# Kernel optimization log

Hardware: AMD Instinct MI355X
Metric: run time of the kernel (lower is better)

The kernel has to match this reference:

```python
import jax, jax.numpy as jnp
import numpy as np

DIMS, HEAD = 1024, 16
HD = DIMS // HEAD  # 64
MAX_ITER = 3
B, T = 4, 2048


def _ln(x, w, eps=1e-5):
    # torch LayerNorm with bias=False
    m = jnp.mean(x, axis=-1, keepdims=True)
    v = jnp.var(x, axis=-1, keepdims=True)
    return (x - m) * jax.lax.rsqrt(v + eps) * w


def setup_inputs() -> dict:
    key = jax.random.key(0)
    ks = jax.random.split(key, 10)
    n = lambda k, s: jax.random.normal(k, s, jnp.float32) * 0.02
    z = lambda s: jnp.zeros(s, jnp.float32)
    o = lambda s: jnp.ones(s, jnp.float32)
    return {
        "x": jax.random.normal(ks[0], (B, T, DIMS), jnp.float32),
        "Wq": n(ks[1], (DIMS, DIMS)), "bq": z((DIMS,)),
        "Wk": n(ks[2], (DIMS, DIMS)),
        "Wv": n(ks[3], (DIMS, DIMS)), "bv": z((DIMS,)),
        "Wo": n(ks[4], (DIMS, DIMS)), "bo": z((DIMS,)),
        "lna_w": o((DIMS,)), "lnc_w": o((HD,)), "lnd_w": o((HD,)),
        "Wlq": n(ks[5], (HD, HD)), "blq": z((HD,)),
        "Wlk": n(ks[6], (HD, HD)), "blk": z((HD,)),
        "Wlv": n(ks[7], (HD, HD)), "blv": z((HD,)),
        "temp": jnp.float32(1.0),
        "threshold": jnp.float32(0.01),
        "factor": jnp.float32(0.1),
    }


def reference(x, Wq, bq, Wk, Wv, bv, Wo, bo, lna_w, lnc_w, lnd_w,
              Wlq, blq, Wlk, blk, Wlv, blv, temp, threshold, factor):
    Bn, Tn, D = x.shape
    H, hd = HEAD, HD
    # .item() in torch detaches these params
    temp0 = jax.lax.stop_gradient(temp)
    thr = jax.lax.stop_gradient(threshold)
    fac = jax.lax.stop_gradient(factor)

    scale = hd ** -0.25
    xn = _ln(x, lna_w)
    q = (xn @ Wq.T + bq) * scale
    k = (xn @ Wk.T) * scale  # no bias
    v = xn @ Wv.T + bv
    shp = lambda t: t.reshape(Bn, Tn, H, hd).transpose(0, 2, 1, 3)  # (B,H,T,hd)
    q, k, v = shp(q), shp(k), shp(v)

    # eff_span = min(qcur.shape[1], k.shape[1]) == head dim of (B,H,T,hd)
    E = H
    sm_scale = 1.0 / float(np.sqrt(hd))

    qcur, kcur, vcur = q, k, v
    prev = jnp.zeros_like(q)
    attn_out = jnp.zeros_like(q)
    done = jnp.asarray(False)
    for it in range(MAX_ITER):
        ql = qcur[:, :, :E] @ Wlq.T + blq  # (B,H,E,hd)
        kl = kcur[:, :, :E] @ Wlk.T + blk
        vl = vcur[:, :, :E] @ Wlv.T + blv
        t_it = temp0 + 0.005 * it
        tscale = jnp.where((t_it != 1.0) & (t_it > 0), jax.lax.rsqrt(t_it), 1.0)
        qs = _ln(ql, lnc_w) * tscale
        ks_ = _ln(kl, lnd_w)
        logits = jnp.einsum('bhqd,bhkd->bhqk', qs, ks_) * sm_scale
        ai = jnp.einsum('bhqk,bhkd->bhqd', jax.nn.softmax(logits, axis=-1), vl)
        iter_out = jnp.zeros_like(qcur).at[:, :, :E].set(ai)
        diff = jnp.mean(jnp.abs(iter_out - prev))
        attn_out = jnp.where(done, attn_out, iter_out)  # freeze after break
        done = done | ((diff < thr + fac * diff) & (it > 0))
        prev = iter_out
        qcur = qcur + iter_out
        kcur, vcur = kl, vl

    out = attn_out.transpose(0, 2, 1, 3).reshape(Bn, Tn, D)
    return out @ Wo.T + bo
```

## Files before the change

kernel.cpp:

```cpp
#include <hip/hip_runtime.h>
#include <math.h>

#define WS_XN    0
#define WS_QKVP  65536
#define WS_DIFF  1638400
#define WS_AI1   1638404
#define WS_AI2   1703940
#define WS_WOP   1769476
#define WS_WT    2293764

__device__ __forceinline__ float4 f4zero() { return make_float4(0.f, 0.f, 0.f, 0.f); }
__device__ __forceinline__ float4 f4add(float4 a, float4 b) {
    return make_float4(a.x + b.x, a.y + b.y, a.z + b.z, a.w + b.w);
}
__device__ __forceinline__ float4 f4fma(float s, float4 a, float4 c) {
    return make_float4(fmaf(s, a.x, c.x), fmaf(s, a.y, c.y),
                       fmaf(s, a.z, c.z), fmaf(s, a.w, c.w));
}
__device__ __forceinline__ float dot4acc(float4 a, float4 b, float acc) {
    acc = fmaf(a.x, b.x, acc); acc = fmaf(a.y, b.y, acc);
    acc = fmaf(a.z, b.z, acc); acc = fmaf(a.w, b.w, acc);
    return acc;
}

__device__ __forceinline__ void gemm_lds(const float* __restrict__ ldsA, int tq,
                                         const float* __restrict__ ldsW, int dq,
                                         float acc[4][4]) {
#pragma unroll 8
    for (int k = 0; k < 64; ++k) {
        float4 a4 = *(const float4*)&ldsA[k * 20 + 4 * tq];
        float4 b4 = *(const float4*)&ldsW[k * 64 + 4 * dq];
        float av[4] = { a4.x, a4.y, a4.z, a4.w };
#pragma unroll
        for (int i = 0; i < 4; i++) {
            acc[i][0] = fmaf(av[i], b4.x, acc[i][0]);
            acc[i][1] = fmaf(av[i], b4.y, acc[i][1]);
            acc[i][2] = fmaf(av[i], b4.z, acc[i][2]);
            acc[i][3] = fmaf(av[i], b4.w, acc[i][3]);
        }
    }
}

__global__ __launch_bounds__(256) void k_ln(const float* __restrict__ x,
                                            const float* __restrict__ lna,
                                            const float* __restrict__ Wlq,
                                            const float* __restrict__ Wlk,
                                            const float* __restrict__ Wlv,
                                            float* __restrict__ xn,
                                            float* __restrict__ wt,
                                            float* __restrict__ diffg) {
    if (blockIdx.x >= 64) {
        int m = blockIdx.x - 64;
        const float* W = (m == 0) ? Wlq : (m == 1) ? Wlk : Wlv;
        float* dst = wt + m * 4096;
        for (int i = threadIdx.x; i < 4096; i += 256) {
            int k = i >> 6, d = i & 63;
            dst[i] = W[d * 64 + k];
        }
        return;
    }
    int r = blockIdx.x;
    int b = r >> 4, t = r & 15;
    if (blockIdx.x == 0 && threadIdx.x == 0) diffg[0] = 0.f;
    const float* row = x + (size_t)(b * 2048 + t) * 1024;
    int tid = threadIdx.x;
    float4 xv = *(const float4*)&row[tid * 4];
    float s1 = xv.x + xv.y + xv.z + xv.w;
    float s2 = xv.x * xv.x + xv.y * xv.y + xv.z * xv.z + xv.w * xv.w;
    for (int off = 32; off; off >>= 1) {
        s1 += __shfl_xor(s1, off);
        s2 += __shfl_xor(s2, off);
    }
    __shared__ float ssum[4], ssq[4];
    int wv = tid >> 6, lane = tid & 63;
    if (lane == 0) { ssum[wv] = s1; ssq[wv] = s2; }
    __syncthreads();
    float tot = ssum[0] + ssum[1] + ssum[2] + ssum[3];
    float tq  = ssq[0] + ssq[1] + ssq[2] + ssq[3];
    float m   = tot * (1.0f / 1024.0f);
    float var = tq * (1.0f / 1024.0f) - m * m;
    float rs  = rsqrtf(var + 1e-5f);
    float4 w4 = *(const float4*)&lna[tid * 4];
    float4 o  = make_float4((xv.x - m) * rs * w4.x, (xv.y - m) * rs * w4.y,
                            (xv.z - m) * rs * w4.z, (xv.w - m) * rs * w4.w);
    *(float4*)&xn[r * 1024 + tid * 4] = o;
}

__global__ __launch_bounds__(256) void k_qkv(const float* __restrict__ xn,
                                             const float* __restrict__ Wq,
                                             const float* __restrict__ Wk,
                                             const float* __restrict__ Wv,
                                             float* __restrict__ qkvp) {
    int ct  = blockIdx.x;
    int ksl = blockIdx.y;
    int m   = ct >> 5;
    const float* W = (m == 0) ? Wq : (m == 1) ? Wk : Wv;
    int j0 = (ct & 31) * 32;
    int k0 = ksl * 128;
    __shared__ float At[64][132];
    __shared__ float Bt[32][132];
    int tid = threadIdx.x;
    for (int i = tid; i < 2048; i += 256) {
        int r = i >> 5, kk = (i & 31) << 2;
        *(float4*)&At[r][kk] = *(const float4*)&xn[r * 1024 + k0 + kk];
    }
    for (int i = tid; i < 1024; i += 256) {
        int r = i >> 5, kk = (i & 31) << 2;
        *(float4*)&Bt[r][kk] = *(const float4*)&W[(size_t)(j0 + r) * 1024 + k0 + kk];
    }
    __syncthreads();
    int rg = tid >> 4, cg = tid & 15;
    float acc[4][2];
#pragma unroll
    for (int i = 0; i < 4; i++) { acc[i][0] = 0.f; acc[i][1] = 0.f; }
    for (int k = 0; k < 128; k += 4) {
        float4 b0 = *(float4*)&Bt[cg * 2 + 0][k];
        float4 b1 = *(float4*)&Bt[cg * 2 + 1][k];
#pragma unroll
        for (int i = 0; i < 4; i++) {
            float4 a = *(float4*)&At[rg * 4 + i][k];
            acc[i][0] = dot4acc(a, b0, acc[i][0]);
            acc[i][1] = dot4acc(a, b1, acc[i][1]);
        }
    }
    float* dst = qkvp + (size_t)ksl * 196608;
    int colg = ct * 32 + cg * 2;
#pragma unroll
    for (int i = 0; i < 4; i++) {
        *(float2*)&dst[(rg * 4 + i) * 3072 + colg] = make_float2(acc[i][0], acc[i][1]);
    }
}

__global__ __launch_bounds__(256, 1) void k_iter(
        const float* __restrict__ qkvp, const float* __restrict__ wt,
        const float* __restrict__ bq,  const float* __restrict__ bv,
        const float* __restrict__ lnc, const float* __restrict__ lnd,
        const float* __restrict__ blq, const float* __restrict__ blk_,
        const float* __restrict__ blv, const float* __restrict__ temp,
        float* __restrict__ ai1g, float* __restrict__ ai2g,
        float* __restrict__ diffg) {
    __shared__ __align__(16) float wS[12288];
    __shared__ __align__(16) float qcT[64 * 20];
    __shared__ __align__(16) float kcT[64 * 20];
    __shared__ __align__(16) float vcT[64 * 20];
    __shared__ __align__(16) float qsR[16 * 68];
    __shared__ __align__(16) float ksR[16 * 68];
    __shared__ __align__(16) float vlR[16 * 68];
    __shared__ float dred[4];

    int tid  = threadIdx.x;
    int b    = blockIdx.x >> 4, h = blockIdx.x & 15;
    int wv   = tid >> 6, lane = tid & 63;
    float tempv = temp[0];

    int tq = lane >> 4, dq = lane & 15;
    int t2 = tid >> 4,  u  = tid & 15;
    int rowi2 = b * 16 + t2, col2 = h * 64 + u * 4;

#pragma unroll
    for (int j = 0; j < 12; ++j) {
        int idx = (tid + j * 256) * 4;
        *(float4*)&wS[idx] = *(const float4*)&wt[idx];
    }

    {
        const float SCALE = 0.35355339059327378f;
        const float* P = qkvp + rowi2 * 3072 + col2;
        float4 q4 = f4zero(), k4 = f4zero(), v4 = f4zero();
#pragma unroll
        for (int sl = 0; sl < 8; sl++) {
            const float* Ps = P + (size_t)sl * 196608;
            q4 = f4add(q4, *(const float4*)&Ps[0]);
            k4 = f4add(k4, *(const float4*)&Ps[1024]);
            v4 = f4add(v4, *(const float4*)&Ps[2048]);
        }
        float4 bq4 = *(const float4*)&bq[col2];
        float4 bv4 = *(const float4*)&bv[col2];
        float qv[4] = { (q4.x + bq4.x) * SCALE, (q4.y + bq4.y) * SCALE,
                        (q4.z + bq4.z) * SCALE, (q4.w + bq4.w) * SCALE };
        float kv[4] = { k4.x * SCALE, k4.y * SCALE, k4.z * SCALE, k4.w * SCALE };
        float vv[4] = { v4.x + bv4.x, v4.y + bv4.y, v4.z + bv4.z, v4.w + bv4.w };
#pragma unroll
        for (int c = 0; c < 4; c++) {
            qcT[(u * 4 + c) * 20 + t2] = qv[c];
            kcT[(u * 4 + c) * 20 + t2] = kv[c];
            vcT[(u * 4 + c) * 20 + t2] = vv[c];
        }
    }
    __syncthreads();

    float4 ai0 = f4zero();
    float  dlocal = 0.f;

#pragma unroll 1
    for (int it = 0; it < 3; ++it) {
        float t_it = tempv + 0.005f * (float)it;
        float tsc  = (t_it != 1.0f && t_it > 0.0f) ? rsqrtf(t_it) : 1.0f;

        if (wv == 0) {
            float acc[4][4];
#pragma unroll
            for (int i = 0; i < 4; i++)
#pragma unroll
                for (int j = 0; j < 4; j++) acc[i][j] = 0.f;
            gemm_lds(qcT, tq, wS, dq, acc);
            float4 bb = *(const float4*)&blq[4 * dq];
            float4 lw = *(const float4*)&lnc[4 * dq];
#pragma unroll
            for (int i = 0; i < 4; i++) {
                acc[i][0] += bb.x; acc[i][1] += bb.y;
                acc[i][2] += bb.z; acc[i][3] += bb.w;
                float s1 = acc[i][0] + acc[i][1] + acc[i][2] + acc[i][3];
                float s2 = acc[i][0]*acc[i][0] + acc[i][1]*acc[i][1]
                         + acc[i][2]*acc[i][2] + acc[i][3]*acc[i][3];
                for (int off = 8; off; off >>= 1) {
                    s1 += __shfl_xor(s1, off); s2 += __shfl_xor(s2, off);
                }
                float m  = s1 * (1.0f / 64.0f);
                float vr = s2 * (1.0f / 64.0f) - m * m;
                float rs = rsqrtf(vr + 1e-5f) * tsc;
                float4 o = make_float4((acc[i][0] - m) * rs * lw.x,
                                       (acc[i][1] - m) * rs * lw.y,
                                       (acc[i][2] - m) * rs * lw.z,
                                       (acc[i][3] - m) * rs * lw.w);
                *(float4*)&qsR[(4 * tq + i) * 68 + 4 * dq] = o;
            }
        } else if (wv == 1) {
            float acc[4][4];
#pragma unroll
            for (int i = 0; i < 4; i++)
#pragma unroll
                for (int j = 0; j < 4; j++) acc[i][j] = 0.f;
            gemm_lds(kcT, tq, wS + 4096, dq, acc);
            float4 bb = *(const float4*)&blk_[4 * dq];
#pragma unroll
            for (int i = 0; i < 4; i++) {
                acc[i][0] += bb.x; acc[i][1] += bb.y;
                acc[i][2] += bb.z; acc[i][3] += bb.w;
            }
#pragma unroll
            for (int j = 0; j < 4; j++) {
                float4 cv = make_float4(acc[0][j], acc[1][j], acc[2][j], acc[3][j]);
                *(float4*)&kcT[(4 * dq + j) * 20 + 4 * tq] = cv;
            }
            float4 lw = *(const float4*)&lnd[4 * dq];
#pragma unroll
            for (int i = 0; i < 4; i++) {
                float s1 = acc[i][0] + acc[i][1] + acc[i][2] + acc[i][3];
                float s2 = acc[i][0]*acc[i][0] + acc[i][1]*acc[i][1]
                         + acc[i][2]*acc[i][2] + acc[i][3]*acc[i][3];
                for (int off = 8; off; off >>= 1) {
                    s1 += __shfl_xor(s1, off); s2 += __shfl_xor(s2, off);
                }
                float m  = s1 * (1.0f / 64.0f);
                float vr = s2 * (1.0f / 64.0f) - m * m;
                float rs = rsqrtf(vr + 1e-5f);
                float4 o = make_float4((acc[i][0] - m) * rs * lw.x,
                                       (acc[i][1] - m) * rs * lw.y,
                                       (acc[i][2] - m) * rs * lw.z,
                                       (acc[i][3] - m) * rs * lw.w);
                *(float4*)&ksR[(4 * tq + i) * 68 + 4 * dq] = o;
            }
        } else if (wv == 2) {
            float acc[4][4];
#pragma unroll
            for (int i = 0; i < 4; i++)
#pragma unroll
                for (int j = 0; j < 4; j++) acc[i][j] = 0.f;
            gemm_lds(vcT, tq, wS + 8192, dq, acc);
            float4 bb = *(const float4*)&blv[4 * dq];
#pragma unroll
            for (int i = 0; i < 4; i++) {
                acc[i][0] += bb.x; acc[i][1] += bb.y;
                acc[i][2] += bb.z; acc[i][3] += bb.w;
                *(float4*)&vlR[(4 * tq + i) * 68 + 4 * dq] =
                    make_float4(acc[i][0], acc[i][1], acc[i][2], acc[i][3]);
            }
#pragma unroll
            for (int j = 0; j < 4; j++) {
                float4 cv = make_float4(acc[0][j], acc[1][j], acc[2][j], acc[3][j]);
                *(float4*)&vcT[(4 * dq + j) * 20 + 4 * tq] = cv;
            }
        }
        __syncthreads();

        float lg = 0.f;
#pragma unroll
        for (int c = 0; c < 16; ++c) {
            float4 a4 = *(float4*)&qsR[t2 * 68 + 4 * c];
            float4 b4 = *(float4*)&ksR[u  * 68 + 4 * c];
            lg = dot4acc(a4, b4, lg);
        }
        lg *= 0.125f;
        float mx = lg;
        for (int off = 8; off; off >>= 1) mx = fmaxf(mx, __shfl_xor(mx, off));
        float e = __expf(lg - mx);
        float sm = e;
        for (int off = 8; off; off >>= 1) sm += __shfl_xor(sm, off);
        float p = e / sm;

        float4 ai = f4zero();
        int gbase = lane & 48;
#pragma unroll
        for (int tk = 0; tk < 16; ++tk) {
            float pk = __shfl(p, gbase + tk);
            ai = f4fma(pk, *(float4*)&vlR[tk * 68 + 4 * u], ai);
        }

        if (it == 0) {
            ai0 = ai;
        } else if (it == 1) {
            dlocal = fabsf(ai.x - ai0.x) + fabsf(ai.y - ai0.y) +
                     fabsf(ai.z - ai0.z) + fabsf(ai.w - ai0.w);
            *(float4*)&ai1g[rowi2 * 1024 + col2] = ai;
        } else {
            *(float4*)&ai2g[rowi2 * 1024 + col2] = ai;
        }
        qcT[(4 * u + 0) * 20 + t2] += ai.x;
        qcT[(4 * u + 1) * 20 + t2] += ai.y;
        qcT[(4 * u + 2) * 20 + t2] += ai.z;
        qcT[(4 * u + 3) * 20 + t2] += ai.w;
        __syncthreads();
    }

    float ds = dlocal;
    for (int off = 32; off; off >>= 1) ds += __shfl_xor(ds, off);
    if (lane == 0) dred[wv] = ds;
    __syncthreads();
    if (tid == 0) atomicAdd(diffg, dred[0] + dred[1] + dred[2] + dred[3]);
}

__global__ __launch_bounds__(256) void k_wo(const float* __restrict__ ai1g,
                                            const float* __restrict__ ai2g,
                                            const float* __restrict__ diffg,
                                            const float* __restrict__ thrp,
                                            const float* __restrict__ facp,
                                            const float* __restrict__ Wo,
                                            float* __restrict__ wop) {
    float diff = diffg[0] * (1.0f / 8388608.0f);
    const float* A = (diff < thrp[0] + facp[0] * diff) ? ai1g : ai2g;
    int jt  = blockIdx.x;
    int ksl = blockIdx.y;
    int k0  = ksl * 128;
    __shared__ float At[64][132];
    __shared__ float Bt[32][132];
    int tid = threadIdx.x;
    for (int i = tid; i < 2048; i += 256) {
        int r = i >> 5, kk = (i & 31) << 2;
        *(float4*)&At[r][kk] = *(const float4*)&A[r * 1024 + k0 + kk];
    }
    for (int i = tid; i < 1024; i += 256) {
        int r = i >> 5, kk = (i & 31) << 2;
        *(float4*)&Bt[r][kk] = *(const float4*)&Wo[(size_t)(jt * 32 + r) * 1024 + k0 + kk];
    }
    __syncthreads();
    int rg = tid >> 4, cg = tid & 15;
    float acc[4][2];
#pragma unroll
    for (int i = 0; i < 4; i++) { acc[i][0] = 0.f; acc[i][1] = 0.f; }
    for (int k = 0; k < 128; k += 4) {
        float4 b0 = *(float4*)&Bt[cg * 2 + 0][k];
        float4 b1 = *(float4*)&Bt[cg * 2 + 1][k];
#pragma unroll
        for (int i = 0; i < 4; i++) {
            float4 a = *(float4*)&At[rg * 4 + i][k];
            acc[i][0] = dot4acc(a, b0, acc[i][0]);
            acc[i][1] = dot4acc(a, b1, acc[i][1]);
        }
    }
    float* dst = wop + (size_t)ksl * 65536;
    int colg = jt * 32 + cg * 2;
#pragma unroll
    for (int i = 0; i < 4; i++) {
        *(float2*)&dst[(rg * 4 + i) * 1024 + colg] = make_float2(acc[i][0], acc[i][1]);
    }
}

__global__ __launch_bounds__(256) void k_bo(const float* __restrict__ bo,
                                            const float* __restrict__ wop,
                                            float* __restrict__ out) {
    int row = blockIdx.x;
    int tid = threadIdx.x;
    int b = row >> 11, t = row & 2047;
    float4 o = *(const float4*)&bo[tid * 4];
    if (t < 16) {
        int ri = b * 16 + t;
#pragma unroll
        for (int s = 0; s < 8; s++) {
            float4 p = *(const float4*)&wop[(size_t)s * 65536 + ri * 1024 + tid * 4];
            o = f4add(o, p);
        }
    }
    *(float4*)&out[(size_t)row * 1024 + tid * 4] = o;
}

extern "C" void kernel_launch(void* const* d_in, const int* in_sizes, int n_in,
                              void* d_out, int out_size, void* d_ws, size_t ws_size,
                              hipStream_t stream) {
    (void)in_sizes; (void)n_in; (void)out_size; (void)ws_size;
    const float* x    = (const float*)d_in[0];
    const float* Wq   = (const float*)d_in[1];
    const float* bq   = (const float*)d_in[2];
    const float* Wk   = (const float*)d_in[3];
    const float* Wv   = (const float*)d_in[4];
    const float* bv   = (const float*)d_in[5];
    const float* Wo   = (const float*)d_in[6];
    const float* bo   = (const float*)d_in[7];
    const float* lna  = (const float*)d_in[8];
    const float* lnc  = (const float*)d_in[9];
    const float* lnd  = (const float*)d_in[10];
    const float* Wlq  = (const float*)d_in[11];
    const float* blq  = (const float*)d_in[12];
    const float* Wlk  = (const float*)d_in[13];
    const float* blk_ = (const float*)d_in[14];
    const float* Wlv  = (const float*)d_in[15];
    const float* blv  = (const float*)d_in[16];
    const float* temp = (const float*)d_in[17];
    const float* thr  = (const float*)d_in[18];
    const float* fac  = (const float*)d_in[19];
    float* ws  = (float*)d_ws;
    float* out = (float*)d_out;

    k_ln  <<<67, 256, 0, stream>>>(x, lna, Wlq, Wlk, Wlv,
                                   ws + WS_XN, ws + WS_WT, ws + WS_DIFF);
    k_qkv <<<dim3(96, 8), 256, 0, stream>>>(ws + WS_XN, Wq, Wk, Wv, ws + WS_QKVP);
    k_iter<<<64, 256, 0, stream>>>(ws + WS_QKVP, ws + WS_WT, bq, bv, lnc, lnd,
                                   blq, blk_, blv, temp,
                                   ws + WS_AI1, ws + WS_AI2, ws + WS_DIFF);
    k_wo  <<<dim3(32, 8), 256, 0, stream>>>(ws + WS_AI1, ws + WS_AI2, ws + WS_DIFF,
                                            thr, fac, Wo, ws + WS_WOP);
    k_bo  <<<8192, 256, 0, stream>>>(bo, ws + WS_WOP, out);
}
```

Measured before the change: 160.2 us.

## Move bias-only output fill into k_iter spare blocks and shrink k_bo

The bias-only fill of output rows t>=16 moves out of k_bo into 8128 extra blocks of k_iter, which otherwise runs only 64 blocks. These blocks overlap with the 64 attention blocks and can hide the large output write. k_bo now launches only 64 blocks to reduce the wop partials for the 16 live rows. It also skips redundant LDS write-backs on the last iteration, keeps q in registers, and raises launch bounds to 2 waves per EU, which may constrain registers.

```diff
diff --git a/kernel.cpp b/kernel.cpp
--- a/kernel.cpp
+++ b/kernel.cpp
@@ -131,12 +131,13 @@
     }
 }
 
-__global__ __launch_bounds__(256, 1) void k_iter(
+__global__ __launch_bounds__(256, 2) void k_iter(
         const float* __restrict__ qkvp, const float* __restrict__ wt,
         const float* __restrict__ bq,  const float* __restrict__ bv,
         const float* __restrict__ lnc, const float* __restrict__ lnd,
         const float* __restrict__ blq, const float* __restrict__ blk_,
         const float* __restrict__ blv, const float* __restrict__ temp,
+        const float* __restrict__ bo,  float* __restrict__ out,
         float* __restrict__ ai1g, float* __restrict__ ai2g,
         float* __restrict__ diffg) {
     __shared__ __align__(16) float wS[12288];
@@ -149,6 +150,16 @@
     __shared__ float dred[4];
 
     int tid  = threadIdx.x;
+
+    if (blockIdx.x >= 64) {
+        int i2 = blockIdx.x - 64;
+        int bb = i2 / 2032;
+        int tt = 16 + (i2 - bb * 2032);
+        float4 o = *(const float4*)&bo[tid * 4];
+        *(float4*)&out[(size_t)(bb * 2048 + tt) * 1024 + tid * 4] = o;
+        return;
+    }
+
     int b    = blockIdx.x >> 4, h = blockIdx.x & 15;
     int wv   = tid >> 6, lane = tid & 63;
     float tempv = temp[0];
@@ -163,6 +174,7 @@
         *(float4*)&wS[idx] = *(const float4*)&wt[idx];
     }
 
+    float4 qreg;
     {
         const float SCALE = 0.35355339059327378f;
         const float* P = qkvp + rowi2 * 3072 + col2;
@@ -176,10 +188,11 @@
         }
         float4 bq4 = *(const float4*)&bq[col2];
         float4 bv4 = *(const float4*)&bv[col2];
-        float qv[4] = { (q4.x + bq4.x) * SCALE, (q4.y + bq4.y) * SCALE,
-                        (q4.z + bq4.z) * SCALE, (q4.w + bq4.w) * SCALE };
+        qreg = make_float4((q4.x + bq4.x) * SCALE, (q4.y + bq4.y) * SCALE,
+                           (q4.z + bq4.z) * SCALE, (q4.w + bq4.w) * SCALE);
         float kv[4] = { k4.x * SCALE, k4.y * SCALE, k4.z * SCALE, k4.w * SCALE };
         float vv[4] = { v4.x + bv4.x, v4.y + bv4.y, v4.z + bv4.z, v4.w + bv4.w };
+        float qv[4] = { qreg.x, qreg.y, qreg.z, qreg.w };
 #pragma unroll
         for (int c = 0; c < 4; c++) {
             qcT[(u * 4 + c) * 20 + t2] = qv[c];
@@ -238,10 +251,12 @@
                 acc[i][0] += bb.x; acc[i][1] += bb.y;
                 acc[i][2] += bb.z; acc[i][3] += bb.w;
             }
-#pragma unroll
-            for (int j = 0; j < 4; j++) {
-                float4 cv = make_float4(acc[0][j], acc[1][j], acc[2][j], acc[3][j]);
-                *(float4*)&kcT[(4 * dq + j) * 20 + 4 * tq] = cv;
+            if (it < 2) {
+#pragma unroll
+                for (int j = 0; j < 4; j++) {
+                    float4 cv = make_float4(acc[0][j], acc[1][j], acc[2][j], acc[3][j]);
+                    *(float4*)&kcT[(4 * dq + j) * 20 + 4 * tq] = cv;
+                }
             }
             float4 lw = *(const float4*)&lnd[4 * dq];
 #pragma unroll
@@ -276,10 +291,12 @@
                 *(float4*)&vlR[(4 * tq + i) * 68 + 4 * dq] =
                     make_float4(acc[i][0], acc[i][1], acc[i][2], acc[i][3]);
             }
-#pragma unroll
-            for (int j = 0; j < 4; j++) {
-                float4 cv = make_float4(acc[0][j], acc[1][j], acc[2][j], acc[3][j]);
-                *(float4*)&vcT[(4 * dq + j) * 20 + 4 * tq] = cv;
+            if (it < 2) {
+#pragma unroll
+                for (int j = 0; j < 4; j++) {
+                    float4 cv = make_float4(acc[0][j], acc[1][j], acc[2][j], acc[3][j]);
+                    *(float4*)&vcT[(4 * dq + j) * 20 + 4 * tq] = cv;
+                }
             }
         }
         __syncthreads();
@@ -316,10 +333,13 @@
         } else {
             *(float4*)&ai2g[rowi2 * 1024 + col2] = ai;
         }
-        qcT[(4 * u + 0) * 20 + t2] += ai.x;
-        qcT[(4 * u + 1) * 20 + t2] += ai.y;
-        qcT[(4 * u + 2) * 20 + t2] += ai.z;
-        qcT[(4 * u + 3) * 20 + t2] += ai.w;
+        if (it < 2) {
+            qreg = f4add(qreg, ai);
+            qcT[(4 * u + 0) * 20 + t2] = qreg.x;
+            qcT[(4 * u + 1) * 20 + t2] = qreg.y;
+            qcT[(4 * u + 2) * 20 + t2] = qreg.z;
+            qcT[(4 * u + 3) * 20 + t2] = qreg.w;
+        }
         __syncthreads();
     }
 
@@ -379,19 +399,16 @@
 __global__ __launch_bounds__(256) void k_bo(const float* __restrict__ bo,
                                             const float* __restrict__ wop,
                                             float* __restrict__ out) {
-    int row = blockIdx.x;
+    int ri  = blockIdx.x;
     int tid = threadIdx.x;
-    int b = row >> 11, t = row & 2047;
+    int b = ri >> 4, t = ri & 15;
     float4 o = *(const float4*)&bo[tid * 4];
-    if (t < 16) {
-        int ri = b * 16 + t;
-#pragma unroll
-        for (int s = 0; s < 8; s++) {
-            float4 p = *(const float4*)&wop[(size_t)s * 65536 + ri * 1024 + tid * 4];
-            o = f4add(o, p);
-        }
-    }
-    *(float4*)&out[(size_t)row * 1024 + tid * 4] = o;
+#pragma unroll
+    for (int s = 0; s < 8; s++) {
+        float4 p = *(const float4*)&wop[(size_t)s * 65536 + ri * 1024 + tid * 4];
+        o = f4add(o, p);
+    }
+    *(float4*)&out[(size_t)(b * 2048 + t) * 1024 + tid * 4] = o;
 }
 
 extern "C" void kernel_launch(void* const* d_in, const int* in_sizes, int n_in,
@@ -424,10 +441,11 @@
     k_ln  <<<67, 256, 0, stream>>>(x, lna, Wlq, Wlk, Wlv,
                                    ws + WS_XN, ws + WS_WT, ws + WS_DIFF);
     k_qkv <<<dim3(96, 8), 256, 0, stream>>>(ws + WS_XN, Wq, Wk, Wv, ws + WS_QKVP);
-    k_iter<<<64, 256, 0, stream>>>(ws + WS_QKVP, ws + WS_WT, bq, bv, lnc, lnd,
-                                   blq, blk_, blv, temp,
-                                   ws + WS_AI1, ws + WS_AI2, ws + WS_DIFF);
+    k_iter<<<64 + 8128, 256, 0, stream>>>(ws + WS_QKVP, ws + WS_WT, bq, bv,
+                                          lnc, lnd, blq, blk_, blv, temp,
+                                          bo, out,
+                                          ws + WS_AI1, ws + WS_AI2, ws + WS_DIFF);
     k_wo  <<<dim3(32, 8), 256, 0, stream>>>(ws + WS_AI1, ws + WS_AI2, ws + WS_DIFF,
                                             thr, fac, Wo, ws + WS_WOP);
-    k_bo  <<<8192, 256, 0, stream>>>(bo, ws + WS_WOP, out);
-}
+    k_bo  <<<64, 256, 0, stream>>>(bo, ws + WS_WOP, out);
+}
```

After: 159.2 us. No clear change (-0.6%).
